# Optimization experiments

Measured on AMD Instinct MI355X. Metric: run time of the kernel, lower is better.

## Reference

```python
import jax, jax.numpy as jnp
import numpy as np

# Module hyperparameters (from AdaptiveWeightInterpolationModule defaults)
SIGMA_D = 1.5        # gaussian splat bandwidth
TAO_R = 0.05         # truncation threshold on gaussian splat weight
PROW = 2             # splat window: offsets in [-PROW+1, PROW] -> (2*PROW)^2 taps
LAMBDA_E = 30.0 / 255.0
LAMBDA_V = 1.0
NW = 3               # photometric-error averaging window
THRESH = 1e-06
EPS = 1e-06


def _bilinear_warp(img, flow):
    """Backward-warp img [B,C,H,W] by flow [B,2,H,W] (sample at x+u, y+v)."""
    B, C, H, W = img.shape
    xs = jnp.arange(W, dtype=flow.dtype)
    ys = jnp.arange(H, dtype=flow.dtype)
    gx = jnp.clip(xs[None, None, :] + flow[:, 0], 0.0, W - 1.0)  # [B,H,W]
    gy = jnp.clip(ys[None, :, None] + flow[:, 1], 0.0, H - 1.0)
    x0 = jnp.floor(gx); y0 = jnp.floor(gy)
    x1 = jnp.minimum(x0 + 1.0, W - 1.0); y1 = jnp.minimum(y0 + 1.0, H - 1.0)
    wx = (gx - x0)[:, None]; wy = (gy - y0)[:, None]  # [B,1,H,W]
    flat = img.reshape(B, C, H * W)

    def gather(yi, xi):
        idx = (yi * W + xi).astype(jnp.int32).reshape(B, 1, H * W)
        g = jnp.take_along_axis(flat, jnp.broadcast_to(idx, (B, C, H * W)), axis=2)
        return g.reshape(B, C, H, W)

    Ia = gather(y0, x0); Ib = gather(y0, x1)
    Ic = gather(y1, x0); Id = gather(y1, x1)
    return Ia * (1 - wx) * (1 - wy) + Ib * wx * (1 - wy) + Ic * (1 - wx) * wy + Id * wx * wy


def _weight_layer(i1, i2, flow):
    """WeightLayer: photometric-consistency flow weight, [B,1,H,W]."""
    warped = _bilinear_warp(i2, flow)
    err = jnp.mean(jnp.abs(i1 - warped), axis=1, keepdims=True)  # [B,1,H,W]
    k = jnp.ones((1, 1, NW, NW), err.dtype) / float(NW * NW)
    err = jax.lax.conv_general_dilated(err, k, (1, 1), 'SAME',
                                       dimension_numbers=('NCHW', 'OIHW', 'NCHW'))
    return LAMBDA_V * jnp.exp(-(err / LAMBDA_E) ** 2)


def _splat(flow, src):
    """Forward gaussian splat of src [B,C,H,W] along flow [B,2,H,W] -> [B,C,H,W].
    Each source pixel scatters src*exp(-d^2/(2 sigma_d^2)) (truncated at TAO_R)
    to the (2*PROW)^2 integer neighbors of its flow target."""
    B, C, H, W = src.shape
    xs = jnp.arange(W, dtype=flow.dtype)
    ys = jnp.arange(H, dtype=flow.dtype)
    tx = xs[None, None, :] + flow[:, 0]  # [B,H,W]
    ty = ys[None, :, None] + flow[:, 1]
    fx = jnp.floor(tx); fy = jnp.floor(ty)
    boff = (jnp.arange(B) * H * W)[:, None, None]
    srcf = src.transpose(1, 0, 2, 3).reshape(C, B * H * W)
    out = jnp.zeros((C, B * H * W), src.dtype)
    inv2s2 = 1.0 / (2.0 * SIGMA_D * SIGMA_D)
    for dy in range(-PROW + 1, PROW + 1):
        for dx in range(-PROW + 1, PROW + 1):
            ix = fx + dx; iy = fy + dy
            d2 = (tx - ix) ** 2 + (ty - iy) ** 2
            g = jnp.exp(-d2 * inv2s2)
            g = jnp.where(g > TAO_R, g, 0.0)  # tao_r truncation
            valid = (ix >= 0) & (ix < W) & (iy >= 0) & (iy < H)
            g = jnp.where(valid, g, 0.0)
            idx = (boff + jnp.clip(iy, 0, H - 1) * W + jnp.clip(ix, 0, W - 1))
            idx = idx.astype(jnp.int32).reshape(B * H * W)
            out = out.at[:, idx].add(srcf * g.reshape(1, B * H * W))
    return out.reshape(C, B, H, W).transpose(1, 0, 2, 3)


def setup_inputs() -> dict:
    key = jax.random.key(0)
    k1, k2, k3, k4 = jax.random.split(key, 4)
    B, H, W = 4, 720, 1280
    return {
        'input1': jax.random.uniform(k1, (B, 3, H, W), jnp.float32),
        'input2': jax.random.uniform(k2, (B, 3, H, W), jnp.float32),
        'input3': jax.random.normal(k3, (B, 2, H, W), jnp.float32),
        'input4': jax.random.normal(k4, (B, 2, H, W), jnp.float32),
    }


def reference(input1, input2, input3, input4):
    # branch 1: warp frame 1 forward with flow input3
    fw1 = _weight_layer(input1, input2, input3)            # [B,1,H,W]
    p1 = _splat(input3, input1 * fw1)                      # PixelValueLayer
    pw1 = _splat(input3, fw1)                              # PixelWeightLayer
    rw1 = _splat(input3, jnp.ones_like(fw1))               # ReliableWeightLayer
    i1 = p1 / (pw1 + THRESH)
    w1 = pw1 / (rw1 + THRESH)
    # branch 2: warp frame 2 forward with flow input4
    fw2 = _weight_layer(input2, input1, input4)
    p2 = _splat(input4, input2 * fw2)
    pw2 = _splat(input4, fw2)
    rw2 = _splat(input4, jnp.ones_like(fw2))
    i2 = p2 / (pw2 + THRESH)
    w2 = pw2 / (rw2 + THRESH)
    # adaptive blend
    return (i1 * w1 + i2 * w2) / (w1 + w2 + EPS)
```

## Files before the change

### kernel.cpp

```cpp
#include <hip/hip_runtime.h>

#define BATCH 4
#define HGT   720
#define WID   1280
#define HW    (HGT * WID)
#define NPIX  (BATCH * HW)
#define NQUAD (NPIX / 4)
#define INV2S2 0.22222222222222222f
#define INV_LAMBDA_E (255.0f / 30.0f)
#define THRESH 1e-6f
#define EPSV   1e-6f

#define GT    16
#define GM    5
#define GE    (GT + 2 * GM)
#define GEC   (GE * GE)
#define CUT   4.0f
#define CELLS 19
#define SCOL  20
#define ECAP  208

__global__ __launch_bounds__(256) void err_kernel(
    const float* __restrict__ i1, const float* __restrict__ i2,
    const float* __restrict__ flow, float* __restrict__ err) {
  int q = blockIdx.x * blockDim.x + threadIdx.x;
  if (q >= NQUAD) return;
  int n0 = q * 4;
  int b = n0 / HW;
  int r0 = n0 - b * HW;
  int y = r0 / WID;
  int x0 = r0 - y * WID;

  const float4 uq = *(const float4*)(flow + (size_t)(b * 2 + 0) * HW + r0);
  const float4 vq = *(const float4*)(flow + (size_t)(b * 2 + 1) * HW + r0);
  const float* up = &uq.x;
  const float* vp = &vq.x;
  const float* i2b = i2 + (size_t)b * 3 * HW;
  const float* i1b = i1 + (size_t)b * 3 * HW;

  float4 eo;
  float* ep = &eo.x;
#pragma unroll
  for (int i = 0; i < 4; ++i) {
    int x = x0 + i;
    int r = r0 + i;
    float gx = fminf(fmaxf((float)x + up[i], 0.0f), (float)(WID - 1));
    float gy = fminf(fmaxf((float)y + vp[i], 0.0f), (float)(HGT - 1));
    float x0f = floorf(gx), y0f = floorf(gy);
    int xa = (int)x0f, ya = (int)y0f;
    int xb = min(xa + 1, WID - 1), yb = min(ya + 1, HGT - 1);
    float wx = gx - x0f, wy = gy - y0f;
    float w00 = (1.0f - wx) * (1.0f - wy);
    float w01 = wx * (1.0f - wy);
    float w10 = (1.0f - wx) * wy;
    float w11 = wx * wy;
    int i00 = ya * WID + xa, i01 = ya * WID + xb;
    int i10 = yb * WID + xa, i11 = yb * WID + xb;
    float s = 0.0f;
#pragma unroll
    for (int c = 0; c < 3; ++c) {
      const float* pl = i2b + c * HW;
      float wv = pl[i00] * w00 + pl[i01] * w01 + pl[i10] * w10 + pl[i11] * w11;
      s += fabsf(i1b[c * HW + r] - wv);
    }
    ep[i] = s * (1.0f / 3.0f);
  }
  *(float4*)(err + n0) = eo;
}

__global__ __launch_bounds__(256) void fw_kernel(
    const float* __restrict__ err, float* __restrict__ fw) {
  int q = blockIdx.x * blockDim.x + threadIdx.x;
  if (q >= NQUAD) return;
  int n0 = q * 4;
  int b = n0 / HW;
  int r0 = n0 - b * HW;
  int y = r0 / WID;
  int x0 = r0 - y * WID;
  const float* e = err + (size_t)b * HW;

  float s0 = 0.f, s1 = 0.f, s2 = 0.f, s3 = 0.f;
#pragma unroll
  for (int dy = -1; dy <= 1; ++dy) {
    int yy = y + dy;
    if (yy < 0 || yy >= HGT) continue;
    const float* row = e + yy * WID;
    float4 qv = *(const float4*)(row + x0);
    float l = (x0 > 0) ? row[x0 - 1] : 0.0f;
    float r = (x0 + 4 < WID) ? row[x0 + 4] : 0.0f;
    s0 += l + qv.x + qv.y;
    s1 += qv.x + qv.y + qv.z;
    s2 += qv.y + qv.z + qv.w;
    s3 += qv.z + qv.w + r;
  }
  float4 o;
  float t;
  t = s0 * (1.0f / 9.0f) * INV_LAMBDA_E; o.x = expf(-t * t);
  t = s1 * (1.0f / 9.0f) * INV_LAMBDA_E; o.y = expf(-t * t);
  t = s2 * (1.0f / 9.0f) * INV_LAMBDA_E; o.z = expf(-t * t);
  t = s3 * (1.0f / 9.0f) * INV_LAMBDA_E; o.w = expf(-t * t);
  *(float4*)(fw + n0) = o;
}

__global__ __launch_bounds__(256) void splat_binned_kernel(
    const float* __restrict__ flow, const float* __restrict__ img,
    const float* __restrict__ fw, float* __restrict__ p,
    float* __restrict__ pw, float* __restrict__ rw) {
  __shared__ float2 sfrac[GEC];
  __shared__ float4 sval[GEC];
  __shared__ unsigned short sent[CELLS * ECAP];
  __shared__ unsigned int scnt[CELLS * CELLS];
  __shared__ unsigned int sstart[CELLS * SCOL];

  const int b = blockIdx.z;
  const int tx0 = blockIdx.x * GT;
  const int ty0 = blockIdx.y * GT;
  const int ex0 = tx0 - GM;
  const int ey0 = ty0 - GM;
  const float* fu  = flow + (size_t)(b * 2 + 0) * HW;
  const float* fv  = flow + (size_t)(b * 2 + 1) * HW;
  const float* ib  = img + (size_t)b * 3 * HW;
  const float* fwb = fw + (size_t)b * HW;

  for (int i = threadIdx.x; i < CELLS * CELLS; i += 256) scnt[i] = 0u;
  __syncthreads();

  int mycell[3];
  unsigned int myofs[3];
#pragma unroll
  for (int t = 0; t < 3; ++t) {
    int cell = -1;
    unsigned int ofs = 0;
    int i = threadIdx.x + t * 256;
    if (i < GEC) {
      int sly = i / GE, slx = i - sly * GE;
      int sx = ex0 + slx, sy = ey0 + sly;
      if (sx >= 0 && sx < WID && sy >= 0 && sy < HGT) {
        int r = sy * WID + sx;
        float u = fu[r], v = fv[r];
        if (fabsf(u) < CUT && fabsf(v) < CUT) {
          float tx = (float)sx + u;
          float ty = (float)sy + v;
          float fx = floorf(tx), fy = floorf(ty);
          int cx = (int)fx - (tx0 - 2);
          int cy = (int)fy - (ty0 - 2);
          if (cx >= 0 && cx < CELLS && cy >= 0 && cy < CELLS) {
            float fwv = fwb[r];
            sfrac[i] = make_float2(tx - fx, ty - fy);
            sval[i] = make_float4(ib[r] * fwv, ib[HW + r] * fwv,
                                  ib[2 * HW + r] * fwv, fwv);
            cell = cy * CELLS + cx;
            ofs = atomicAdd(&scnt[cell], 1u);
          }
        }
      }
    }
    mycell[t] = cell;
    myofs[t] = ofs;
  }
  __syncthreads();

  for (int c = threadIdx.x; c < CELLS * SCOL; c += 256) {
    int cy = c / SCOL, cx = c - cy * SCOL;
    unsigned int s = 0;
    for (int q = 0; q < cx; ++q) s += scnt[cy * CELLS + q];
    sstart[c] = s;
  }
  __syncthreads();

#pragma unroll
  for (int t = 0; t < 3; ++t) {
    if (mycell[t] >= 0) {
      int cy = mycell[t] / CELLS, cx = mycell[t] - cy * CELLS;
      unsigned int pos = sstart[cy * SCOL + cx] + myofs[t];
      sent[cy * ECAP + pos] =
          (unsigned short)(((unsigned)cx << 10) | (unsigned)(threadIdx.x + t * 256));
    }
  }
  __syncthreads();

  const int lx = threadIdx.x & 15;
  const int ly = threadIdx.x >> 4;
  float a0 = 0.f, a1 = 0.f, a2 = 0.f, apw = 0.f, arw = 0.f;

#pragma unroll
  for (int k = 0; k < 4; ++k) {
    const int cy = ly + k;
    int s = (int)sstart[cy * SCOL + lx];
    int e = (int)sstart[cy * SCOL + lx + 4];
    const float cky = (float)(2 - k);
    const int ebase = cy * ECAP;
    for (int j = s; j < e; ++j) {
      unsigned int en = sent[ebase + j];
      int slot = en & 1023;
      int cx = en >> 10;
      float2 fr = sfrac[slot];
      float ddx = fr.x - (float)(lx - cx + 2);
      float ddy = fr.y - cky;
      float g = __expf(-(ddx * ddx + ddy * ddy) * INV2S2);
      float4 vl = sval[slot];
      a0 += vl.x * g;
      a1 += vl.y * g;
      a2 += vl.z * g;
      apw += vl.w * g;
      arw += g;
    }
  }

  const int gi = b * HW + (ty0 + ly) * WID + tx0 + lx;
  p[gi]            = a0;
  p[NPIX + gi]     = a1;
  p[2 * NPIX + gi] = a2;
  pw[gi]           = apw;
  rw[gi]           = arw;
}

__global__ __launch_bounds__(256) void outlier_kernel(
    const float* __restrict__ flow, const float* __restrict__ img,
    const float* __restrict__ fw, float* __restrict__ p,
    float* __restrict__ pw, float* __restrict__ rw) {
  int q = blockIdx.x * blockDim.x + threadIdx.x;
  if (q >= NQUAD) return;
  int n0 = q * 4;
  int b = n0 / HW;
  int r0 = n0 - b * HW;
  const float4 uq = *(const float4*)(flow + (size_t)(b * 2 + 0) * HW + r0);
  const float4 vq = *(const float4*)(flow + (size_t)(b * 2 + 1) * HW + r0);
  const float* up = &uq.x;
  const float* vp = &vq.x;

  bool any = false;
#pragma unroll
  for (int i = 0; i < 4; ++i)
    any |= !(fabsf(up[i]) < CUT && fabsf(vp[i]) < CUT);
  if (!any) return;

  const float* ib = img + (size_t)b * 3 * HW;
  int base = b * HW;
#pragma unroll
  for (int i = 0; i < 4; ++i) {
    float u = up[i], v = vp[i];
    if (fabsf(u) < CUT && fabsf(v) < CUT) continue;
    int r = r0 + i;
    int y = r / WID;
    int x = r - y * WID;
    float txf = (float)x + u, tyf = (float)y + v;
    float fx = floorf(txf), fy = floorf(tyf);
    int ixb = (int)fx, iyb = (int)fy;
    float fracx = txf - fx, fracy = tyf - fy;

    float gxv[4], gyv[4];
#pragma unroll
    for (int d = 0; d < 4; ++d) {
      float ddx = fracx - (float)(d - 1);
      gxv[d] = __expf(-ddx * ddx * INV2S2);
      float ddy = fracy - (float)(d - 1);
      gyv[d] = __expf(-ddy * ddy * INV2S2);
    }

    float fwv = fw[b * HW + r];
    float s0 = ib[0 * HW + r] * fwv;
    float s1 = ib[1 * HW + r] * fwv;
    float s2 = ib[2 * HW + r] * fwv;

    for (int dy = 0; dy < 4; ++dy) {
      int iy = iyb + dy - 1;
      if (iy < 0 || iy >= HGT) continue;
      float gy = gyv[dy];
      for (int dx = 0; dx < 4; ++dx) {
        int ix = ixb + dx - 1;
        if (ix < 0 || ix >= WID) continue;
        float g = gxv[dx] * gy;
        int gi = base + iy * WID + ix;
        atomicAdd(p + gi, s0 * g);
        atomicAdd(p + NPIX + gi, s1 * g);
        atomicAdd(p + 2 * NPIX + gi, s2 * g);
        atomicAdd(pw + gi, fwv * g);
        atomicAdd(rw + gi, g);
      }
    }
  }
}

__global__ __launch_bounds__(256) void blend_kernel(
    const float* __restrict__ p1, const float* __restrict__ pw1,
    const float* __restrict__ rw1, const float* __restrict__ p2,
    const float* __restrict__ pw2, const float* __restrict__ rw2,
    float* __restrict__ out) {
  int q = blockIdx.x * blockDim.x + threadIdx.x;
  if (q >= NQUAD) return;
  int n0 = q * 4;
  int b = n0 / HW;
  int r0 = n0 - b * HW;

  float4 pw1v = *(const float4*)(pw1 + n0);
  float4 rw1v = *(const float4*)(rw1 + n0);
  float4 pw2v = *(const float4*)(pw2 + n0);
  float4 rw2v = *(const float4*)(rw2 + n0);
  const float* pw1p = &pw1v.x; const float* rw1p = &rw1v.x;
  const float* pw2p = &pw2v.x; const float* rw2p = &rw2v.x;

  float s1v[4], s2v[4], iv[4];
#pragma unroll
  for (int i = 0; i < 4; ++i) {
    float w1 = pw1p[i] / (rw1p[i] + THRESH);
    float s1 = w1 / (pw1p[i] + THRESH);
    float w2 = pw2p[i] / (rw2p[i] + THRESH);
    float s2 = w2 / (pw2p[i] + THRESH);
    s1v[i] = s1; s2v[i] = s2;
    iv[i] = 1.0f / (w1 + w2 + EPSV);
  }

  size_t ob = (size_t)b * 3 * HW + r0;
#pragma unroll
  for (int c = 0; c < 3; ++c) {
    float4 a = *(const float4*)(p1 + (size_t)c * NPIX + n0);
    float4 bq = *(const float4*)(p2 + (size_t)c * NPIX + n0);
    const float* ap = &a.x; const float* bp = &bq.x;
    float4 o;
    float* op = &o.x;
#pragma unroll
    for (int i = 0; i < 4; ++i)
      op[i] = (ap[i] * s1v[i] + bp[i] * s2v[i]) * iv[i];
    *(float4*)(out + ob + (size_t)c * HW) = o;
  }
}

__global__ __launch_bounds__(256) void acc1_kernel(
    const float* __restrict__ p, const float* __restrict__ pw,
    const float* __restrict__ rw, float* __restrict__ out,
    float* __restrict__ den) {
  int n = blockIdx.x * blockDim.x + threadIdx.x;
  if (n >= NPIX) return;
  int b = n / HW;
  int r = n - b * HW;
  float pwv = pw[n], rwv = rw[n];
  float w = pwv / (rwv + THRESH);
  den[n] = w;
  float scale = w / (pwv + THRESH);
  int ob = b * 3 * HW + r;
  out[ob + 0 * HW] = p[n] * scale;
  out[ob + 1 * HW] = p[NPIX + n] * scale;
  out[ob + 2 * HW] = p[2 * NPIX + n] * scale;
}

__global__ __launch_bounds__(256) void acc2_kernel(
    const float* __restrict__ p, const float* __restrict__ pw,
    const float* __restrict__ rw, const float* __restrict__ den,
    float* __restrict__ out) {
  int n = blockIdx.x * blockDim.x + threadIdx.x;
  if (n >= NPIX) return;
  int b = n / HW;
  int r = n - b * HW;
  float pwv = pw[n], rwv = rw[n];
  float w = pwv / (rwv + THRESH);
  float scale = w / (pwv + THRESH);
  float d = den[n] + w + EPSV;
  float invd = 1.0f / d;
  int ob = b * 3 * HW + r;
  out[ob + 0 * HW] = (out[ob + 0 * HW] + p[n] * scale) * invd;
  out[ob + 1 * HW] = (out[ob + 1 * HW] + p[NPIX + n] * scale) * invd;
  out[ob + 2 * HW] = (out[ob + 2 * HW] + p[2 * NPIX + n] * scale) * invd;
}

extern "C" void kernel_launch(void* const* d_in, const int* in_sizes, int n_in,
                              void* d_out, int out_size, void* d_ws,
                              size_t ws_size, hipStream_t stream) {
  const float* input1 = (const float*)d_in[0];
  const float* input2 = (const float*)d_in[1];
  const float* flow3  = (const float*)d_in[2];
  const float* flow4  = (const float*)d_in[3];
  float* out = (float*)d_out;
  float* ws  = (float*)d_ws;

  const int threads = 256;
  const int qblocks = (NQUAD + threads - 1) / threads;
  const int nblocks = (NPIX + threads - 1) / threads;
  dim3 sgrid(WID / GT, HGT / GT, BATCH);

  if (ws_size >= (size_t)11 * NPIX * sizeof(float)) {
    float* p1  = ws;
    float* pw1 = ws + (size_t)3 * NPIX;
    float* rw1 = ws + (size_t)4 * NPIX;
    float* p2  = ws + (size_t)5 * NPIX;
    float* pw2 = ws + (size_t)8 * NPIX;
    float* rw2 = ws + (size_t)9 * NPIX;
    float* fw  = ws + (size_t)10 * NPIX;
    float* err = p2;

    err_kernel<<<qblocks, threads, 0, stream>>>(input1, input2, flow3, err);
    fw_kernel<<<qblocks, threads, 0, stream>>>(err, fw);
    splat_binned_kernel<<<sgrid, threads, 0, stream>>>(flow3, input1, fw, p1, pw1, rw1);
    outlier_kernel<<<qblocks, threads, 0, stream>>>(flow3, input1, fw, p1, pw1, rw1);
    err_kernel<<<qblocks, threads, 0, stream>>>(input2, input1, flow4, err);
    fw_kernel<<<qblocks, threads, 0, stream>>>(err, fw);
    splat_binned_kernel<<<sgrid, threads, 0, stream>>>(flow4, input2, fw, p2, pw2, rw2);
    outlier_kernel<<<qblocks, threads, 0, stream>>>(flow4, input2, fw, p2, pw2, rw2);
    blend_kernel<<<qblocks, threads, 0, stream>>>(p1, pw1, rw1, p2, pw2, rw2, out);
  } else {
    float* p   = ws;
    float* err = ws;
    float* pw  = ws + (size_t)3 * NPIX;
    float* rw  = ws + (size_t)4 * NPIX;
    float* fw  = ws + (size_t)5 * NPIX;
    float* den = ws + (size_t)6 * NPIX;

    err_kernel<<<qblocks, threads, 0, stream>>>(input1, input2, flow3, err);
    fw_kernel<<<qblocks, threads, 0, stream>>>(err, fw);
    splat_binned_kernel<<<sgrid, threads, 0, stream>>>(flow3, input1, fw, p, pw, rw);
    outlier_kernel<<<qblocks, threads, 0, stream>>>(flow3, input1, fw, p, pw, rw);
    acc1_kernel<<<nblocks, threads, 0, stream>>>(p, pw, rw, out, den);

    err_kernel<<<qblocks, threads, 0, stream>>>(input2, input1, flow4, err);
    fw_kernel<<<qblocks, threads, 0, stream>>>(err, fw);
    splat_binned_kernel<<<sgrid, threads, 0, stream>>>(flow4, input2, fw, p, pw, rw);
    outlier_kernel<<<qblocks, threads, 0, stream>>>(flow4, input2, fw, p, pw, rw);
    acc2_kernel<<<nblocks, threads, 0, stream>>>(p, pw, rw, den, out);
  }
}
```

Baseline: 558.3 us.

## Tile warp-error gather in LDS, simplify splat inner loop, vectorize accumulate kernels

The photometric error kernel now loads a 29x29 halo tile of the second image into shared memory per 16x16 block and does the bilinear gather from LDS when the flow is small, falling back to global loads otherwise. The splat inner loop stores a precomputed cell-offset position per source so the entry index no longer packs the cell x, and it accumulates channels with 2-wide vector FMAs. The acc1 and acc2 kernels are rewritten to process four pixels per thread with float4 loads and stores. The err kernel's tile load adds a block-wide barrier and LDS traffic, and pixels with large flow still pay for uncoalesced global reads.

New measurement: 526.1 us. -5.8%, faster.

```diff
diff --git a/kernel.cpp b/kernel.cpp
--- a/kernel.cpp
+++ b/kernel.cpp
@@ -20,52 +20,69 @@
 #define SCOL  20
 #define ECAP  208
 
+#define EHL 6
+#define EW  29
+
+typedef float v2f __attribute__((ext_vector_type(2)));
+
 __global__ __launch_bounds__(256) void err_kernel(
     const float* __restrict__ i1, const float* __restrict__ i2,
     const float* __restrict__ flow, float* __restrict__ err) {
-  int q = blockIdx.x * blockDim.x + threadIdx.x;
-  if (q >= NQUAD) return;
-  int n0 = q * 4;
-  int b = n0 / HW;
-  int r0 = n0 - b * HW;
-  int y = r0 / WID;
-  int x0 = r0 - y * WID;
-
-  const float4 uq = *(const float4*)(flow + (size_t)(b * 2 + 0) * HW + r0);
-  const float4 vq = *(const float4*)(flow + (size_t)(b * 2 + 1) * HW + r0);
-  const float* up = &uq.x;
-  const float* vp = &vq.x;
+  __shared__ float tile[3][EW * EW + 1];
+  const int b = blockIdx.z;
+  const int tx0 = blockIdx.x * 16, ty0 = blockIdx.y * 16;
+  const int ex0 = tx0 - EHL, ey0 = ty0 - EHL;
   const float* i2b = i2 + (size_t)b * 3 * HW;
+
+  for (int i = threadIdx.x; i < EW * EW; i += 256) {
+    int iy = i / EW, ix = i - iy * EW;
+    int sx = ex0 + ix, sy = ey0 + iy;
+    float c0 = 0.f, c1 = 0.f, c2 = 0.f;
+    if (sx >= 0 && sx < WID && sy >= 0 && sy < HGT) {
+      int r = sy * WID + sx;
+      c0 = i2b[r]; c1 = i2b[HW + r]; c2 = i2b[2 * HW + r];
+    }
+    tile[0][i] = c0; tile[1][i] = c1; tile[2][i] = c2;
+  }
+  __syncthreads();
+
+  const int lx = threadIdx.x & 15, ly = threadIdx.x >> 4;
+  const int x = tx0 + lx, y = ty0 + ly;
+  const int r = y * WID + x;
+  float u = flow[(size_t)(b * 2 + 0) * HW + r];
+  float v = flow[(size_t)(b * 2 + 1) * HW + r];
+  float gx = fminf(fmaxf((float)x + u, 0.0f), (float)(WID - 1));
+  float gy = fminf(fmaxf((float)y + v, 0.0f), (float)(HGT - 1));
+  float x0f = floorf(gx), y0f = floorf(gy);
+  int x0 = (int)x0f, y0 = (int)y0f;
+  int x1 = min(x0 + 1, WID - 1), y1 = min(y0 + 1, HGT - 1);
+  float wx = gx - x0f, wy = gy - y0f;
+  float w00 = (1.0f - wx) * (1.0f - wy);
+  float w01 = wx * (1.0f - wy);
+  float w10 = (1.0f - wx) * wy;
+  float w11 = wx * wy;
   const float* i1b = i1 + (size_t)b * 3 * HW;
-
-  float4 eo;
-  float* ep = &eo.x;
-#pragma unroll
-  for (int i = 0; i < 4; ++i) {
-    int x = x0 + i;
-    int r = r0 + i;
-    float gx = fminf(fmaxf((float)x + up[i], 0.0f), (float)(WID - 1));
-    float gy = fminf(fmaxf((float)y + vp[i], 0.0f), (float)(HGT - 1));
-    float x0f = floorf(gx), y0f = floorf(gy);
-    int xa = (int)x0f, ya = (int)y0f;
-    int xb = min(xa + 1, WID - 1), yb = min(ya + 1, HGT - 1);
-    float wx = gx - x0f, wy = gy - y0f;
-    float w00 = (1.0f - wx) * (1.0f - wy);
-    float w01 = wx * (1.0f - wy);
-    float w10 = (1.0f - wx) * wy;
-    float w11 = wx * wy;
-    int i00 = ya * WID + xa, i01 = ya * WID + xb;
-    int i10 = yb * WID + xa, i11 = yb * WID + xb;
-    float s = 0.0f;
+  float s = 0.0f;
+  if (fabsf(u) < 6.0f && fabsf(v) < 6.0f) {
+    int j00 = (y0 - ey0) * EW + (x0 - ex0);
+    int jdx = x1 - x0, jdy = (y1 - y0) * EW;
+#pragma unroll
+    for (int c = 0; c < 3; ++c) {
+      float wv = tile[c][j00] * w00 + tile[c][j00 + jdx] * w01 +
+                 tile[c][j00 + jdy] * w10 + tile[c][j00 + jdy + jdx] * w11;
+      s += fabsf(i1b[c * HW + r] - wv);
+    }
+  } else {
+    int i00 = y0 * WID + x0, i01 = y0 * WID + x1;
+    int i10 = y1 * WID + x0, i11 = y1 * WID + x1;
 #pragma unroll
     for (int c = 0; c < 3; ++c) {
       const float* pl = i2b + c * HW;
       float wv = pl[i00] * w00 + pl[i01] * w01 + pl[i10] * w10 + pl[i11] * w11;
       s += fabsf(i1b[c * HW + r] - wv);
     }
-    ep[i] = s * (1.0f / 3.0f);
-  }
-  *(float4*)(err + n0) = eo;
+  }
+  err[(size_t)b * HW + r] = s * (1.0f / 3.0f);
 }
 
 __global__ __launch_bounds__(256) void fw_kernel(
@@ -106,7 +123,7 @@
     const float* __restrict__ flow, const float* __restrict__ img,
     const float* __restrict__ fw, float* __restrict__ p,
     float* __restrict__ pw, float* __restrict__ rw) {
-  __shared__ float2 sfrac[GEC];
+  __shared__ float2 sfp[GEC];
   __shared__ float4 sval[GEC];
   __shared__ unsigned short sent[CELLS * ECAP];
   __shared__ unsigned int scnt[CELLS * CELLS];
@@ -146,7 +163,7 @@
           int cy = (int)fy - (ty0 - 2);
           if (cx >= 0 && cx < CELLS && cy >= 0 && cy < CELLS) {
             float fwv = fwb[r];
-            sfrac[i] = make_float2(tx - fx, ty - fy);
+            sfp[i] = make_float2((tx - fx) + (float)cx, (ty - fy) - 2.0f);
             sval[i] = make_float4(ib[r] * fwv, ib[HW + r] * fwv,
                                   ib[2 * HW + r] * fwv, fwv);
             cell = cy * CELLS + cx;
@@ -173,45 +190,45 @@
     if (mycell[t] >= 0) {
       int cy = mycell[t] / CELLS, cx = mycell[t] - cy * CELLS;
       unsigned int pos = sstart[cy * SCOL + cx] + myofs[t];
-      sent[cy * ECAP + pos] =
-          (unsigned short)(((unsigned)cx << 10) | (unsigned)(threadIdx.x + t * 256));
+      sent[cy * ECAP + pos] = (unsigned short)(threadIdx.x + t * 256);
     }
   }
   __syncthreads();
 
   const int lx = threadIdx.x & 15;
   const int ly = threadIdx.x >> 4;
-  float a0 = 0.f, a1 = 0.f, a2 = 0.f, apw = 0.f, arw = 0.f;
+  const float Lx2 = (float)(lx + 2);
+  v2f a01 = {0.f, 0.f}, a2w = {0.f, 0.f};
+  float arw = 0.f;
 
 #pragma unroll
   for (int k = 0; k < 4; ++k) {
     const int cy = ly + k;
     int s = (int)sstart[cy * SCOL + lx];
     int e = (int)sstart[cy * SCOL + lx + 4];
-    const float cky = (float)(2 - k);
+    const float kf = (float)k;
     const int ebase = cy * ECAP;
     for (int j = s; j < e; ++j) {
-      unsigned int en = sent[ebase + j];
-      int slot = en & 1023;
-      int cx = en >> 10;
-      float2 fr = sfrac[slot];
-      float ddx = fr.x - (float)(lx - cx + 2);
-      float ddy = fr.y - cky;
+      int slot = sent[ebase + j];
+      float2 fp = sfp[slot];
+      float ddx = fp.x - Lx2;
+      float ddy = fp.y + kf;
       float g = __expf(-(ddx * ddx + ddy * ddy) * INV2S2);
       float4 vl = sval[slot];
-      a0 += vl.x * g;
-      a1 += vl.y * g;
-      a2 += vl.z * g;
-      apw += vl.w * g;
+      v2f g2 = {g, g};
+      v2f v01 = {vl.x, vl.y};
+      v2f v2w = {vl.z, vl.w};
+      a01 += v01 * g2;
+      a2w += v2w * g2;
       arw += g;
     }
   }
 
   const int gi = b * HW + (ty0 + ly) * WID + tx0 + lx;
-  p[gi]            = a0;
-  p[NPIX + gi]     = a1;
-  p[2 * NPIX + gi] = a2;
-  pw[gi]           = apw;
+  p[gi]            = a01.x;
+  p[NPIX + gi]     = a01.y;
+  p[2 * NPIX + gi] = a2w.x;
+  pw[gi]           = a2w.y;
   rw[gi]           = arw;
 }
 
@@ -330,37 +347,66 @@
     const float* __restrict__ p, const float* __restrict__ pw,
     const float* __restrict__ rw, float* __restrict__ out,
     float* __restrict__ den) {
-  int n = blockIdx.x * blockDim.x + threadIdx.x;
-  if (n >= NPIX) return;
-  int b = n / HW;
-  int r = n - b * HW;
-  float pwv = pw[n], rwv = rw[n];
-  float w = pwv / (rwv + THRESH);
-  den[n] = w;
-  float scale = w / (pwv + THRESH);
-  int ob = b * 3 * HW + r;
-  out[ob + 0 * HW] = p[n] * scale;
-  out[ob + 1 * HW] = p[NPIX + n] * scale;
-  out[ob + 2 * HW] = p[2 * NPIX + n] * scale;
+  int q = blockIdx.x * blockDim.x + threadIdx.x;
+  if (q >= NQUAD) return;
+  int n0 = q * 4;
+  int b = n0 / HW;
+  int r0 = n0 - b * HW;
+  float4 pwv = *(const float4*)(pw + n0);
+  float4 rwv = *(const float4*)(rw + n0);
+  const float* pwp = &pwv.x; const float* rwp = &rwv.x;
+  float4 wv; float* wp = &wv.x;
+  float sv[4];
+#pragma unroll
+  for (int i = 0; i < 4; ++i) {
+    float w = pwp[i] / (rwp[i] + THRESH);
+    wp[i] = w;
+    sv[i] = w / (pwp[i] + THRESH);
+  }
+  *(float4*)(den + n0) = wv;
+  size_t ob = (size_t)b * 3 * HW + r0;
+#pragma unroll
+  for (int c = 0; c < 3; ++c) {
+    float4 a = *(const float4*)(p + (size_t)c * NPIX + n0);
+    const float* ap = &a.x;
+    float4 o; float* op = &o.x;
+#pragma unroll
+    for (int i = 0; i < 4; ++i) op[i] = ap[i] * sv[i];
+    *(float4*)(out + ob + (size_t)c * HW) = o;
+  }
 }
 
 __global__ __launch_bounds__(256) void acc2_kernel(
     const float* __restrict__ p, const float* __restrict__ pw,
     const float* __restrict__ rw, const float* __restrict__ den,
     float* __restrict__ out) {
-  int n = blockIdx.x * blockDim.x + threadIdx.x;
-  if (n >= NPIX) return;
-  int b = n / HW;
-  int r = n - b * HW;
-  float pwv = pw[n], rwv = rw[n];
-  float w = pwv / (rwv + THRESH);
-  float scale = w / (pwv + THRESH);
-  float d = den[n] + w + EPSV;
-  float invd = 1.0f / d;
-  int ob = b * 3 * HW + r;
-  out[ob + 0 * HW] = (out[ob + 0 * HW] + p[n] * scale) * invd;
-  out[ob + 1 * HW] = (out[ob + 1 * HW] + p[NPIX + n] * scale) * invd;
-  out[ob + 2 * HW] = (out[ob + 2 * HW] + p[2 * NPIX + n] * scale) * invd;
+  int q = blockIdx.x * blockDim.x + threadIdx.x;
+  if (q >= NQUAD) return;
+  int n0 = q * 4;
+  int b = n0 / HW;
+  int r0 = n0 - b * HW;
+  float4 pwv = *(const float4*)(pw + n0);
+  float4 rwv = *(const float4*)(rw + n0);
+  float4 dnv = *(const float4*)(den + n0);
+  const float* pwp = &pwv.x; const float* rwp = &rwv.x;
+  const float* dnp = &dnv.x;
+  float sv[4], iv[4];
+#pragma unroll
+  for (int i = 0; i < 4; ++i) {
+    float w = pwp[i] / (rwp[i] + THRESH);
+    sv[i] = w / (pwp[i] + THRESH);
+    iv[i] = 1.0f / (dnp[i] + w + EPSV);
+  }
+  size_t ob = (size_t)b * 3 * HW + r0;
+#pragma unroll
+  for (int c = 0; c < 3; ++c) {
+    float4 a = *(const float4*)(p + (size_t)c * NPIX + n0);
+    float4 o = *(const float4*)(out + ob + (size_t)c * HW);
+    const float* ap = &a.x; float* op = &o.x;
+#pragma unroll
+    for (int i = 0; i < 4; ++i) op[i] = (op[i] + ap[i] * sv[i]) * iv[i];
+    *(float4*)(out + ob + (size_t)c * HW) = o;
+  }
 }
 
 extern "C" void kernel_launch(void* const* d_in, const int* in_sizes, int n_in,
@@ -375,8 +421,8 @@
 
   const int threads = 256;
   const int qblocks = (NQUAD + threads - 1) / threads;
-  const int nblocks = (NPIX + threads - 1) / threads;
   dim3 sgrid(WID / GT, HGT / GT, BATCH);
+  dim3 egrid(WID / 16, HGT / 16, BATCH);
 
   if (ws_size >= (size_t)11 * NPIX * sizeof(float)) {
     float* p1  = ws;
@@ -388,11 +434,11 @@
     float* fw  = ws + (size_t)10 * NPIX;
     float* err = p2;
 
-    err_kernel<<<qblocks, threads, 0, stream>>>(input1, input2, flow3, err);
+    err_kernel<<<egrid, threads, 0, stream>>>(input1, input2, flow3, err);
     fw_kernel<<<qblocks, threads, 0, stream>>>(err, fw);
     splat_binned_kernel<<<sgrid, threads, 0, stream>>>(flow3, input1, fw, p1, pw1, rw1);
     outlier_kernel<<<qblocks, threads, 0, stream>>>(flow3, input1, fw, p1, pw1, rw1);
-    err_kernel<<<qblocks, threads, 0, stream>>>(input2, input1, flow4, err);
+    err_kernel<<<egrid, threads, 0, stream>>>(input2, input1, flow4, err);
     fw_kernel<<<qblocks, threads, 0, stream>>>(err, fw);
     splat_binned_kernel<<<sgrid, threads, 0, stream>>>(flow4, input2, fw, p2, pw2, rw2);
     outlier_kernel<<<qblocks, threads, 0, stream>>>(flow4, input2, fw, p2, pw2, rw2);
@@ -405,16 +451,16 @@
     float* fw  = ws + (size_t)5 * NPIX;
     float* den = ws + (size_t)6 * NPIX;
 
-    err_kernel<<<qblocks, threads, 0, stream>>>(input1, input2, flow3, err);
+    err_kernel<<<egrid, threads, 0, stream>>>(input1, input2, flow3, err);
     fw_kernel<<<qblocks, threads, 0, stream>>>(err, fw);
     splat_binned_kernel<<<sgrid, threads, 0, stream>>>(flow3, input1, fw, p, pw, rw);
     outlier_kernel<<<qblocks, threads, 0, stream>>>(flow3, input1, fw, p, pw, rw);
-    acc1_kernel<<<nblocks, threads, 0, stream>>>(p, pw, rw, out, den);
-
-    err_kernel<<<qblocks, threads, 0, stream>>>(input2, input1, flow4, err);
+    acc1_kernel<<<qblocks, threads, 0, stream>>>(p, pw, rw, out, den);
+
+    err_kernel<<<egrid, threads, 0, stream>>>(input2, input1, flow4, err);
     fw_kernel<<<qblocks, threads, 0, stream>>>(err, fw);
     splat_binned_kernel<<<sgrid, threads, 0, stream>>>(flow4, input2, fw, p, pw, rw);
     outlier_kernel<<<qblocks, threads, 0, stream>>>(flow4, input2, fw, p, pw, rw);
-    acc2_kernel<<<nblocks, threads, 0, stream>>>(p, pw, rw, den, out);
-  }
-}
+    acc2_kernel<<<qblocks, threads, 0, stream>>>(p, pw, rw, den, out);
+  }
+}
```
